# Optimization experiments

Measured on AMD Instinct MI355X. Metric: run time of the kernel, lower is better.

Reference implementation:

```python
import jax, jax.numpy as jnp
import numpy as np

IN, HID, OUT = 64, 256, 64
B, NSTEPS, DELAY = 256, 1024, 20


def setup_inputs() -> dict:
    key = jax.random.key(0)
    ks = jax.random.split(key, 8)
    s = 0.05
    return {
        "input": jax.random.normal(ks[0], (B, NSTEPS, IN), jnp.float32),
        "W_ih_x": jax.random.normal(ks[1], (4 * HID, IN), jnp.float32) * s,
        "W_ih_fb": jax.random.normal(ks[2], (4 * HID, OUT), jnp.float32) * s,
        "W_hh": jax.random.normal(ks[3], (4 * HID, HID), jnp.float32) * s,
        "b_ih": jax.random.normal(ks[4], (4 * HID,), jnp.float32) * s,
        "b_hh": jax.random.normal(ks[5], (4 * HID,), jnp.float32) * s,
        "W_out": jax.random.normal(ks[6], (OUT, HID), jnp.float32) * s,
        "b_out": jax.random.normal(ks[7], (OUT,), jnp.float32) * s,
        "delay": DELAY,
    }


def reference(input, W_ih_x, W_ih_fb, W_hh, b_ih, b_hh, W_out, b_out, delay):
    b, nsteps, _ = input.shape
    H = W_hh.shape[1]
    O = W_out.shape[0]
    # Precompute the input contribution to the gates for all timesteps:
    # gates_t = x_t @ W_ih_x.T + fb @ W_ih_fb.T + h @ W_hh.T + b_ih + b_hh
    xg = jnp.einsum("btd,gd->tbg", input, W_ih_x) + (b_ih + b_hh)  # [T, B, 4H]

    h0 = jnp.zeros((b, H), input.dtype)
    c0 = jnp.zeros((b, H), input.dtype)
    buf0 = jnp.zeros((delay, b, O), input.dtype)  # ring buffer of past outputs
    ptr0 = jnp.zeros((), jnp.int32)

    def step(carry, xg_t):
        h, c, buf, ptr = carry
        fb = buf[ptr]  # output from `delay` steps ago (zeros initially)
        gates = xg_t + fb @ W_ih_fb.T + h @ W_hh.T  # [B, 4H]
        i, f, g, o = jnp.split(gates, 4, axis=-1)  # torch LSTMCell gate order
        c = jax.nn.sigmoid(f) * c + jax.nn.sigmoid(i) * jnp.tanh(g)
        h = jax.nn.sigmoid(o) * jnp.tanh(c)
        out = h @ W_out.T + b_out  # [B, O]
        buf = buf.at[ptr].set(out)
        ptr = (ptr + 1) % delay
        return (h, c, buf, ptr), out

    _, outs = jax.lax.scan(step, (h0, c0, buf0, ptr0), xg)  # outs: [T, B, O]
    return jnp.transpose(outs, (1, 0, 2))  # [B, T, O]
```

## Files before the change

### kernel.cpp

```cpp
#include <hip/hip_runtime.h>


#define BATCH   256
#define TSTEPS  1024
#define IN_DIM  64
#define HID     256
#define OUT_DIM 64
#define DELAY   20
#define CH      8
#define NCH     (TSTEPS / CH)
#define NTHR    512
#define REGP    25

typedef unsigned int u32;
typedef _Float16 half2_t __attribute__((ext_vector_type(2)));

union H2U { u32 u; half2_t h; };
union H1U { unsigned short s; _Float16 h; };

__device__ __forceinline__ u32 pack2(float a, float b) {
    H2U x; x.h = half2_t{(_Float16)a, (_Float16)b}; return x.u;
}
__device__ __forceinline__ unsigned short f16bits(float a) {
    H1U x; x.h = (_Float16)a; return x.s;
}
__device__ __forceinline__ float lo16(u32 u) {
    H1U x; x.s = (unsigned short)(u & 0xffffu); return (float)x.h;
}
__device__ __forceinline__ float hi16(u32 u) {
    H1U x; x.s = (unsigned short)(u >> 16); return (float)x.h;
}
__device__ __forceinline__ float dot2(u32 w, u32 h, float acc) {
    H2U a; a.u = w; H2U b; b.u = h;
    return __builtin_amdgcn_fdot2(a.h, b.h, acc, false);
}
__device__ __forceinline__ float sigm(float x) {
    float e = __expf(-fabsf(x));
    float p = 1.f / (1.f + e);
    return x >= 0.f ? p : 1.f - p;
}
__device__ __forceinline__ float tanh_f(float x) {
    float e = __expf(-2.f * fabsf(x));
    float r = (1.f - e) / (1.f + e);
    return x >= 0.f ? r : -r;
}

#define OFF_WA    0
#define OFF_WB    65536
#define OFF_WC    98304
#define OFF_CB    114688
#define OFF_PART  131072
#define OFF_RING  139264
#define OFF_XF    141824
#define OFF_HG    144000
#define SMEM_BYTES 152192

#define WS_BPK   0
#define WS_WOUT  262144
#define WS_BSUM  294912
#define WS_NEED  299008

__device__ __forceinline__ int orig_row(int gp) {
    return (gp & 3) * 256 + (gp >> 2);
}

__global__ void prepack(const float* __restrict__ Wx,
                        const float* __restrict__ Wfb,
                        const float* __restrict__ Whh,
                        const float* __restrict__ Wout,
                        const float* __restrict__ bih,
                        const float* __restrict__ bhh,
                        uint4* __restrict__ Bpk4,
                        u32* __restrict__ Woutpk,
                        float* __restrict__ bsum_g)
{
    (void)Whh;
    int id = blockIdx.x * 256 + threadIdx.x;
    if (id < 16384) {
        int t = id & 511, rest = id >> 9;
        int kb = rest & 15, j = rest >> 4;
        int r = orig_row(2 * t + j);
        int k0 = kb * 8;
        const float* src = (k0 < 64) ? (Wx + (size_t)r * 64 + k0)
                                     : (Wfb + (size_t)r * 64 + (k0 - 64));
        uint4 v;
        v.x = pack2(src[0], src[1]); v.y = pack2(src[2], src[3]);
        v.z = pack2(src[4], src[5]); v.w = pack2(src[6], src[7]);
        Bpk4[id] = v;
    } else if (id < 16384 + 8192) {
        int s = id - 16384;
        int c = s & 3, o = (s >> 2) & 63, w4 = s >> 8;
        int kp = w4 * 4 + c;
        Woutpk[s] = pack2(Wout[o * HID + 2 * kp], Wout[o * HID + 2 * kp + 1]);
    } else if (id < 16384 + 8192 + 1024) {
        int g = id - 24576;
        int r = orig_row(g);
        bsum_g[g] = bih[r] + bhh[r];
    }
}

__global__ __attribute__((amdgpu_flat_work_group_size(NTHR, NTHR)))
__attribute__((amdgpu_waves_per_eu(2, 2)))
void lstm_persist(const float* __restrict__ input,
                  const float* __restrict__ Whh,
                  const float* __restrict__ bout_g,
                  const uint4* __restrict__ Bpk4,
                  const u32* __restrict__ Woutpk,
                  const float* __restrict__ bsum_g,
                  float* __restrict__ out)
{
    __shared__ alignas(16) unsigned char smem[SMEM_BYTES];
    uint4*          wAl   = (uint4*)(smem + OFF_WA);
    uint2*          wBl   = (uint2*)(smem + OFF_WB);
    u32*            wCl   = (u32*)(smem + OFF_WC);
    u32*            cb32  = (u32*)(smem + OFF_CB);
    unsigned short* part  = (unsigned short*)(smem + OFF_PART);
    unsigned short* ring  = (unsigned short*)(smem + OFF_RING);
    u32*            xfst  = (u32*)(smem + OFF_XF);
    unsigned short* hgs   = (unsigned short*)(smem + OFF_HG);

    const int tid = threadIdx.x;
    const int b   = blockIdx.x;
    const int kq  = tid >> 7;
    const int gl  = tid & 127;

    const float* xin  = input + (size_t)b * TSTEPS * IN_DIM;
    float*       outp = out + (size_t)b * TSTEPS * OUT_DIM;
    const float bo_reg = bout_g[tid & 63];

    u32 wreg[8][REGP];
#pragma unroll
    for (int q = 0; q < 8; ++q) {
        const int r = orig_row(gl * 8 + q);
        const float* wrow = Whh + (size_t)r * HID + kq * 64;
#pragma unroll
        for (int p = 0; p < REGP; ++p) {
            float2 w2 = *(const float2*)(wrow + 2 * p);
            wreg[q][p] = pack2(w2.x, w2.y);
        }
        uint4 av;
        av.x = pack2(wrow[50], wrow[51]); av.y = pack2(wrow[52], wrow[53]);
        av.z = pack2(wrow[54], wrow[55]); av.w = pack2(wrow[56], wrow[57]);
        wAl[q * 512 + tid] = av;
        uint2 bv;
        bv.x = pack2(wrow[58], wrow[59]); bv.y = pack2(wrow[60], wrow[61]);
        wBl[q * 512 + tid] = bv;
        wCl[q * 512 + tid] = pack2(wrow[62], wrow[63]);
    }
    {
        u32* hz = (u32*)hgs;
        hz[tid] = 0u; hz[512 + tid] = 0u; hz[1024 + tid] = 0u; hz[1536 + tid] = 0u;
    }
    __syncthreads();

    float c_state = 0.f;

    auto out_chunk = [&](int tbase) {
        const int lt = tid >> 6, o = tid & 63;
        const int t = tbase + lt;
        const uint4* hrow = (const uint4*)(hgs + (t & 15) * HID);
        const uint4* wp = (const uint4*)Woutpk;
        float a = bo_reg;
        for (int w4 = 0; w4 < 32; ++w4) {
            uint4 wv = wp[w4 * 64 + o];
            uint4 hv = hrow[w4];
            a = dot2(wv.x, hv.x, a); a = dot2(wv.y, hv.y, a);
            a = dot2(wv.z, hv.z, a); a = dot2(wv.w, hv.w, a);
        }
        outp[(size_t)t * OUT_DIM + o] = a;
        ring[(t % DELAY) * 64 + o] = f16bits(a);
    };

#pragma unroll 1
    for (int ch = 0; ch < NCH; ++ch) {
#pragma unroll
        for (int q = 0; q < 8; ++q)
#pragma unroll
            for (int p = 0; p < REGP; ++p)
                asm volatile("" : "+v"(wreg[q][p]));

        const int t0 = ch * CH;
        if (ch > 0) out_chunk(t0 - CH);
        __syncthreads();

        {
            int row = tid >> 6, p = tid & 63;
            int t = t0 + row;
            u32 v;
            if (p < 32) {
                float2 x2 = *(const float2*)(xin + (size_t)t * IN_DIM + 2 * p);
                v = pack2(x2.x, x2.y);
            } else {
                int src = t - DELAY;
                if (src >= 0) {
                    int d = 2 * (p - 32);
                    int sl = src % DELAY;
                    v = (u32)ring[sl * 64 + d] | ((u32)ring[sl * 64 + d + 1] << 16);
                } else v = 0u;
            }
            xfst[row * 68 + p] = v;
        }
        __syncthreads();

        {
            float accA[8], accB[8];
#pragma unroll
            for (int i = 0; i < 8; ++i) { accA[i] = 0.f; accB[i] = 0.f; }
            const uint4* bA = Bpk4 + tid;
            const uint4* bB = Bpk4 + 16 * 512 + tid;
#pragma unroll 1
            for (int kb = 0; kb < 16; ++kb) {
                uint4 wA = bA[kb * 512];
                uint4 wB = bB[kb * 512];
#pragma unroll
                for (int tl = 0; tl < 8; ++tl) {
                    uint4 xv = *(const uint4*)(xfst + tl * 68 + kb * 4);
                    accA[tl] = dot2(wA.x, xv.x, accA[tl]);
                    accA[tl] = dot2(wA.y, xv.y, accA[tl]);
                    accA[tl] = dot2(wA.z, xv.z, accA[tl]);
                    accA[tl] = dot2(wA.w, xv.w, accA[tl]);
                    accB[tl] = dot2(wB.x, xv.x, accB[tl]);
                    accB[tl] = dot2(wB.y, xv.y, accB[tl]);
                    accB[tl] = dot2(wB.z, xv.z, accB[tl]);
                    accB[tl] = dot2(wB.w, xv.w, accB[tl]);
                }
            }
            float2 bs = *(const float2*)(bsum_g + 2 * tid);
#pragma unroll
            for (int tl = 0; tl < 8; ++tl)
                cb32[tl * 512 + tid] = pack2(accA[tl] + bs.x, accB[tl] + bs.y);
        }
        __syncthreads();

#pragma unroll 1
        for (int tl = 0; tl < CH; ++tl) {
            const int t = t0 + tl;
            const u32* hrow = (const u32*)hgs + ((t - 1) & 15) * 128 + kq * 32;

            float acc[8];
            if (kq == 0) {
                uint4 cv = *(const uint4*)(cb32 + tl * 512 + gl * 4);
                acc[0] = lo16(cv.x); acc[1] = hi16(cv.x);
                acc[2] = lo16(cv.y); acc[3] = hi16(cv.y);
                acc[4] = lo16(cv.z); acc[5] = hi16(cv.z);
                acc[6] = lo16(cv.w); acc[7] = hi16(cv.w);
            } else {
#pragma unroll
                for (int q = 0; q < 8; ++q) acc[q] = 0.f;
            }
            {
                uint4 h0 = *(const uint4*)(hrow + 0);
                uint4 h1 = *(const uint4*)(hrow + 4);
                uint4 h2 = *(const uint4*)(hrow + 8);
                uint4 h3 = *(const uint4*)(hrow + 12);
#pragma unroll
                for (int q = 0; q < 8; ++q) {
                    acc[q] = dot2(wreg[q][0],  h0.x, acc[q]);
                    acc[q] = dot2(wreg[q][1],  h0.y, acc[q]);
                    acc[q] = dot2(wreg[q][2],  h0.z, acc[q]);
                    acc[q] = dot2(wreg[q][3],  h0.w, acc[q]);
                    acc[q] = dot2(wreg[q][4],  h1.x, acc[q]);
                    acc[q] = dot2(wreg[q][5],  h1.y, acc[q]);
                    acc[q] = dot2(wreg[q][6],  h1.z, acc[q]);
                    acc[q] = dot2(wreg[q][7],  h1.w, acc[q]);
                    acc[q] = dot2(wreg[q][8],  h2.x, acc[q]);
                    acc[q] = dot2(wreg[q][9],  h2.y, acc[q]);
                    acc[q] = dot2(wreg[q][10], h2.z, acc[q]);
                    acc[q] = dot2(wreg[q][11], h2.w, acc[q]);
                    acc[q] = dot2(wreg[q][12], h3.x, acc[q]);
                    acc[q] = dot2(wreg[q][13], h3.y, acc[q]);
                    acc[q] = dot2(wreg[q][14], h3.z, acc[q]);
                    acc[q] = dot2(wreg[q][15], h3.w, acc[q]);
                }
            }
            {
                uint4 h4 = *(const uint4*)(hrow + 16);
                uint4 h5 = *(const uint4*)(hrow + 20);
                uint4 h6 = *(const uint4*)(hrow + 24);
                uint4 h7 = *(const uint4*)(hrow + 28);
#pragma unroll
                for (int q = 0; q < 8; ++q) {
                    acc[q] = dot2(wreg[q][16], h4.x, acc[q]);
                    acc[q] = dot2(wreg[q][17], h4.y, acc[q]);
                    acc[q] = dot2(wreg[q][18], h4.z, acc[q]);
                    acc[q] = dot2(wreg[q][19], h4.w, acc[q]);
                    acc[q] = dot2(wreg[q][20], h5.x, acc[q]);
                    acc[q] = dot2(wreg[q][21], h5.y, acc[q]);
                    acc[q] = dot2(wreg[q][22], h5.z, acc[q]);
                    acc[q] = dot2(wreg[q][23], h5.w, acc[q]);
                    acc[q] = dot2(wreg[q][24], h6.x, acc[q]);
                    uint4 av = wAl[q * 512 + tid];
                    uint2 bv = wBl[q * 512 + tid];
                    u32   cv = wCl[q * 512 + tid];
                    acc[q] = dot2(av.x, h6.y, acc[q]);
                    acc[q] = dot2(av.y, h6.z, acc[q]);
                    acc[q] = dot2(av.z, h6.w, acc[q]);
                    acc[q] = dot2(av.w, h7.x, acc[q]);
                    acc[q] = dot2(bv.x, h7.y, acc[q]);
                    acc[q] = dot2(bv.y, h7.z, acc[q]);
                    acc[q] = dot2(cv,   h7.w, acc[q]);
                }
            }
            {
                uint4 pw;
                pw.x = pack2(acc[0], acc[1]); pw.y = pack2(acc[2], acc[3]);
                pw.z = pack2(acc[4], acc[5]); pw.w = pack2(acc[6], acc[7]);
                *(uint4*)(part + kq * 1024 + gl * 8) = pw;
            }
            __syncthreads();

            if (tid < 256) {
                float s0 = 0.f, s1 = 0.f, s2 = 0.f, s3 = 0.f;
#pragma unroll
                for (int k = 0; k < 4; ++k) {
                    uint2 rd = *(const uint2*)(part + k * 1024 + tid * 4);
                    s0 += lo16(rd.x); s1 += hi16(rd.x);
                    s2 += lo16(rd.y); s3 += hi16(rd.y);
                }
                c_state = sigm(s1) * c_state + sigm(s0) * tanh_f(s2);
                float hval = sigm(s3) * tanh_f(c_state);
                hgs[(t & 15) * HID + tid] = f16bits(hval);
            }
            __syncthreads();
        }
    }
    out_chunk(TSTEPS - CH);
}

extern "C" void kernel_launch(void* const* d_in, const int* in_sizes, int n_in,
                              void* d_out, int out_size, void* d_ws, size_t ws_size,
                              hipStream_t stream)
{
    (void)in_sizes; (void)n_in; (void)out_size;
    const float* input = (const float*)d_in[0];
    const float* Wx    = (const float*)d_in[1];
    const float* Wfb   = (const float*)d_in[2];
    const float* Whh   = (const float*)d_in[3];
    const float* bih   = (const float*)d_in[4];
    const float* bhh   = (const float*)d_in[5];
    const float* Wo    = (const float*)d_in[6];
    const float* bog   = (const float*)d_in[7];
    float* out = (float*)d_out;

    if (ws_size < (size_t)WS_NEED) return;

    uint4* Bpk4   = (uint4*)((char*)d_ws + WS_BPK);
    u32*   Woutpk = (u32*)((char*)d_ws + WS_WOUT);
    float* bsum_g = (float*)((char*)d_ws + WS_BSUM);

    prepack<<<dim3(100), dim3(256), 0, stream>>>(
        Wx, Wfb, Whh, Wo, bih, bhh, Bpk4, Woutpk, bsum_g);
    lstm_persist<<<dim3(BATCH), dim3(NTHR), 0, stream>>>(
        input, Whh, bog, Bpk4, Woutpk, bsum_g, out);
}
```

Before: 5.031 ms.

## Use MFMA for recurrent and input-gate matmuls with gate-interleaved fragment layout

Replaces the fdot2-based per-thread recurrent matvec and input projection with 16x16x32 f16 MFMA instructions. Recurrent weights are prepacked into MFMA fragment order and held across AGPRs, VGPRs and LDS. The gate layout is arranged so each lane receives all four gates of a unit, which removes the cross-warp partial-sum reduction and one barrier per timestep. The catch is that a batch of one per block uses only one useful column of each 16-wide MFMA, and the pointwise math is duplicated across lanes.

```diff
diff --git a/kernel.cpp b/kernel.cpp
--- a/kernel.cpp
+++ b/kernel.cpp
@@ -10,10 +10,12 @@
 #define CH      8
 #define NCH     (TSTEPS / CH)
 #define NTHR    512
-#define REGP    25
 
 typedef unsigned int u32;
 typedef _Float16 half2_t __attribute__((ext_vector_type(2)));
+typedef _Float16 f16x8 __attribute__((ext_vector_type(8)));
+typedef float    f32x4 __attribute__((ext_vector_type(4)));
+typedef u32      u32x4 __attribute__((ext_vector_type(4)));
 
 union H2U { u32 u; half2_t h; };
 union H1U { unsigned short s; _Float16 h; };
@@ -44,21 +46,23 @@
     float r = (1.f - e) / (1.f + e);
     return x >= 0.f ? r : -r;
 }
-
-#define OFF_WA    0
-#define OFF_WB    65536
-#define OFF_WC    98304
-#define OFF_CB    114688
-#define OFF_PART  131072
-#define OFF_RING  139264
-#define OFF_XF    141824
-#define OFF_HG    144000
-#define SMEM_BYTES 152192
-
-#define WS_BPK   0
-#define WS_WOUT  262144
-#define WS_BSUM  294912
-#define WS_NEED  299008
+__device__ __forceinline__ f32x4 mfma16(u32x4 a, u32x4 b, f32x4 c) {
+    return __builtin_amdgcn_mfma_f32_16x16x32_f16(
+        __builtin_bit_cast(f16x8, a), __builtin_bit_cast(f16x8, b), c, 0, 0, 0);
+}
+
+#define OFF_WLF   0
+#define OFF_CBQ   131072
+#define OFF_RING  147456
+#define OFF_XF    150016
+#define OFF_HG    152192
+#define SMEM_BYTES 160384
+
+#define WS_WHHF  0
+#define WS_BPKF  524288
+#define WS_WOUT  786432
+#define WS_BSUMQ 819200
+#define WS_NEED  823296
 
 __device__ __forceinline__ int orig_row(int gp) {
     return (gp & 3) * 256 + (gp >> 2);
@@ -70,90 +74,104 @@
                         const float* __restrict__ Wout,
                         const float* __restrict__ bih,
                         const float* __restrict__ bhh,
-                        uint4* __restrict__ Bpk4,
+                        uint4* __restrict__ WhhF,
+                        uint4* __restrict__ BpkF,
                         u32* __restrict__ Woutpk,
-                        float* __restrict__ bsum_g)
+                        float4* __restrict__ bsumq)
 {
-    (void)Whh;
     int id = blockIdx.x * 256 + threadIdx.x;
-    if (id < 16384) {
-        int t = id & 511, rest = id >> 9;
-        int kb = rest & 15, j = rest >> 4;
-        int r = orig_row(2 * t + j);
-        int k0 = kb * 8;
-        const float* src = (k0 < 64) ? (Wx + (size_t)r * 64 + k0)
-                                     : (Wfb + (size_t)r * 64 + (k0 - 64));
+    if (id < 32768) {
+        int l = id & 63, ks = (id >> 6) & 7, rb = id >> 9;
+        int r = orig_row(rb * 16 + (l & 15));
+        const float* w = Whh + (size_t)r * HID + ks * 32 + (l >> 4) * 8;
         uint4 v;
-        v.x = pack2(src[0], src[1]); v.y = pack2(src[2], src[3]);
-        v.z = pack2(src[4], src[5]); v.w = pack2(src[6], src[7]);
-        Bpk4[id] = v;
-    } else if (id < 16384 + 8192) {
-        int s = id - 16384;
+        v.x = pack2(w[0], w[1]); v.y = pack2(w[2], w[3]);
+        v.z = pack2(w[4], w[5]); v.w = pack2(w[6], w[7]);
+        WhhF[id] = v;
+    } else if (id < 49152) {
+        int s = id - 32768;
+        int l = s & 63, ks = (s >> 6) & 3, rb = s >> 8;
+        int r = orig_row(rb * 16 + (l & 15));
+        int k0 = ks * 32 + (l >> 4) * 8;
+        float e[8];
+#pragma unroll
+        for (int d = 0; d < 8; ++d) {
+            int k = k0 + d;
+            e[d] = (k < 64) ? Wx[(size_t)r * 64 + k] : Wfb[(size_t)r * 64 + (k - 64)];
+        }
+        uint4 v;
+        v.x = pack2(e[0], e[1]); v.y = pack2(e[2], e[3]);
+        v.z = pack2(e[4], e[5]); v.w = pack2(e[6], e[7]);
+        BpkF[s] = v;
+    } else if (id < 57344) {
+        int s = id - 49152;
         int c = s & 3, o = (s >> 2) & 63, w4 = s >> 8;
         int kp = w4 * 4 + c;
         Woutpk[s] = pack2(Wout[o * HID + 2 * kp], Wout[o * HID + 2 * kp + 1]);
-    } else if (id < 16384 + 8192 + 1024) {
-        int g = id - 24576;
-        int r = orig_row(g);
-        bsum_g[g] = bih[r] + bhh[r];
+    } else if (id < 57600) {
+        int u = id - 57344;
+        float4 bv;
+        bv.x = bih[u]       + bhh[u];
+        bv.y = bih[256 + u] + bhh[256 + u];
+        bv.z = bih[512 + u] + bhh[512 + u];
+        bv.w = bih[768 + u] + bhh[768 + u];
+        bsumq[u] = bv;
     }
 }
 
 __global__ __attribute__((amdgpu_flat_work_group_size(NTHR, NTHR)))
 __attribute__((amdgpu_waves_per_eu(2, 2)))
 void lstm_persist(const float* __restrict__ input,
-                  const float* __restrict__ Whh,
+                  const uint4* __restrict__ WhhF,
+                  const uint4* __restrict__ BpkF,
+                  const u32* __restrict__ Woutpk,
+                  const float4* __restrict__ bsumq,
                   const float* __restrict__ bout_g,
-                  const uint4* __restrict__ Bpk4,
-                  const u32* __restrict__ Woutpk,
-                  const float* __restrict__ bsum_g,
                   float* __restrict__ out)
 {
     __shared__ alignas(16) unsigned char smem[SMEM_BYTES];
-    uint4*          wAl   = (uint4*)(smem + OFF_WA);
-    uint2*          wBl   = (uint2*)(smem + OFF_WB);
-    u32*            wCl   = (u32*)(smem + OFF_WC);
-    u32*            cb32  = (u32*)(smem + OFF_CB);
-    unsigned short* part  = (unsigned short*)(smem + OFF_PART);
+    uint4*          wlf   = (uint4*)(smem + OFF_WLF);
+    uint2*          cbq   = (uint2*)(smem + OFF_CBQ);
     unsigned short* ring  = (unsigned short*)(smem + OFF_RING);
     u32*            xfst  = (u32*)(smem + OFF_XF);
     unsigned short* hgs   = (unsigned short*)(smem + OFF_HG);
 
     const int tid = threadIdx.x;
     const int b   = blockIdx.x;
-    const int kq  = tid >> 7;
-    const int gl  = tid & 127;
+    const int w   = tid >> 6;
+    const int l   = tid & 63;
+    const int kg  = l >> 4;
+    const int col = l & 15;
 
     const float* xin  = input + (size_t)b * TSTEPS * IN_DIM;
     float*       outp = out + (size_t)b * TSTEPS * OUT_DIM;
     const float bo_reg = bout_g[tid & 63];
 
-    u32 wreg[8][REGP];
-#pragma unroll
-    for (int q = 0; q < 8; ++q) {
-        const int r = orig_row(gl * 8 + q);
-        const float* wrow = Whh + (size_t)r * HID + kq * 64;
-#pragma unroll
-        for (int p = 0; p < REGP; ++p) {
-            float2 w2 = *(const float2*)(wrow + 2 * p);
-            wreg[q][p] = pack2(w2.x, w2.y);
-        }
-        uint4 av;
-        av.x = pack2(wrow[50], wrow[51]); av.y = pack2(wrow[52], wrow[53]);
-        av.z = pack2(wrow[54], wrow[55]); av.w = pack2(wrow[56], wrow[57]);
-        wAl[q * 512 + tid] = av;
-        uint2 bv;
-        bv.x = pack2(wrow[58], wrow[59]); bv.y = pack2(wrow[60], wrow[61]);
-        wBl[q * 512 + tid] = bv;
-        wCl[q * 512 + tid] = pack2(wrow[62], wrow[63]);
-    }
+    u32x4 wa[32];
+    u32x4 wv[16];
+#pragma unroll
+    for (int i = 0; i < 32; ++i) {
+        wa[i] = __builtin_bit_cast(u32x4, WhhF[((w * 8 + (i >> 2)) * 8 + (i & 3)) * 64 + l]);
+        asm volatile("" : "+a"(wa[i]));
+    }
+#pragma unroll
+    for (int i = 0; i < 16; ++i) {
+        wv[i] = __builtin_bit_cast(u32x4, WhhF[((w * 8 + (i >> 1)) * 8 + 4 + (i & 1)) * 64 + l]);
+        asm volatile("" : "+v"(wv[i]));
+    }
+#pragma unroll
+    for (int i = 0; i < 16; ++i)
+        wlf[i * 512 + tid] = WhhF[((w * 8 + (i >> 1)) * 8 + 6 + (i & 1)) * 64 + l];
+
     {
         u32* hz = (u32*)hgs;
         hz[tid] = 0u; hz[512 + tid] = 0u; hz[1024 + tid] = 0u; hz[1536 + tid] = 0u;
     }
     __syncthreads();
 
-    float c_state = 0.f;
+    float cst[8];
+#pragma unroll
+    for (int j = 0; j < 8; ++j) cst[j] = 0.f;
 
     auto out_chunk = [&](int tbase) {
         const int lt = tid >> 6, o = tid & 63;
@@ -162,10 +180,10 @@
         const uint4* wp = (const uint4*)Woutpk;
         float a = bo_reg;
         for (int w4 = 0; w4 < 32; ++w4) {
-            uint4 wv = wp[w4 * 64 + o];
+            uint4 wvv = wp[w4 * 64 + o];
             uint4 hv = hrow[w4];
-            a = dot2(wv.x, hv.x, a); a = dot2(wv.y, hv.y, a);
-            a = dot2(wv.z, hv.z, a); a = dot2(wv.w, hv.w, a);
+            a = dot2(wvv.x, hv.x, a); a = dot2(wvv.y, hv.y, a);
+            a = dot2(wvv.z, hv.z, a); a = dot2(wvv.w, hv.w, a);
         }
         outp[(size_t)t * OUT_DIM + o] = a;
         ring[(t % DELAY) * 64 + o] = f16bits(a);
@@ -174,10 +192,9 @@
 #pragma unroll 1
     for (int ch = 0; ch < NCH; ++ch) {
 #pragma unroll
-        for (int q = 0; q < 8; ++q)
-#pragma unroll
-            for (int p = 0; p < REGP; ++p)
-                asm volatile("" : "+v"(wreg[q][p]));
+        for (int i = 0; i < 32; ++i) asm volatile("" : "+a"(wa[i]));
+#pragma unroll
+        for (int i = 0; i < 16; ++i) asm volatile("" : "+v"(wv[i]));
 
         const int t0 = ch * CH;
         if (ch > 0) out_chunk(t0 - CH);
@@ -203,123 +220,76 @@
         __syncthreads();
 
         {
-            float accA[8], accB[8];
-#pragma unroll
-            for (int i = 0; i < 8; ++i) { accA[i] = 0.f; accB[i] = 0.f; }
-            const uint4* bA = Bpk4 + tid;
-            const uint4* bB = Bpk4 + 16 * 512 + tid;
-#pragma unroll 1
-            for (int kb = 0; kb < 16; ++kb) {
-                uint4 wA = bA[kb * 512];
-                uint4 wB = bB[kb * 512];
-#pragma unroll
-                for (int tl = 0; tl < 8; ++tl) {
-                    uint4 xv = *(const uint4*)(xfst + tl * 68 + kb * 4);
-                    accA[tl] = dot2(wA.x, xv.x, accA[tl]);
-                    accA[tl] = dot2(wA.y, xv.y, accA[tl]);
-                    accA[tl] = dot2(wA.z, xv.z, accA[tl]);
-                    accA[tl] = dot2(wA.w, xv.w, accA[tl]);
-                    accB[tl] = dot2(wB.x, xv.x, accB[tl]);
-                    accB[tl] = dot2(wB.y, xv.y, accB[tl]);
-                    accB[tl] = dot2(wB.z, xv.z, accB[tl]);
-                    accB[tl] = dot2(wB.w, xv.w, accB[tl]);
+            const int tc = col & 7;
+            const char* xb_base = (const char*)xfst + tc * 272 + kg * 16;
+#pragma unroll
+            for (int g = 0; g < 2; ++g) {
+                f32x4 ag[4];
+#pragma unroll
+                for (int j = 0; j < 4; ++j) ag[j] = f32x4{0.f, 0.f, 0.f, 0.f};
+#pragma unroll
+                for (int ks = 0; ks < 4; ++ks) {
+                    u32x4 xb = *(const u32x4*)(xb_base + ks * 64);
+#pragma unroll
+                    for (int j = 0; j < 4; ++j) {
+                        const int bb = g * 4 + j;
+                        u32x4 af = __builtin_bit_cast(u32x4,
+                            BpkF[((w * 8 + bb) * 4 + ks) * 64 + l]);
+                        ag[j] = mfma16(af, xb, ag[j]);
+                    }
+                }
+#pragma unroll
+                for (int j = 0; j < 4; ++j) {
+                    const int U = w * 32 + (g * 4 + j) * 4 + kg;
+                    float4 bs = bsumq[U];
+                    if (col < 8) {
+                        uint2 o;
+                        o.x = pack2(ag[j][0] + bs.x, ag[j][1] + bs.y);
+                        o.y = pack2(ag[j][2] + bs.z, ag[j][3] + bs.w);
+                        cbq[U * 8 + col] = o;
+                    }
                 }
             }
-            float2 bs = *(const float2*)(bsum_g + 2 * tid);
-#pragma unroll
-            for (int tl = 0; tl < 8; ++tl)
-                cb32[tl * 512 + tid] = pack2(accA[tl] + bs.x, accB[tl] + bs.y);
         }
         __syncthreads();
 
 #pragma unroll 1
         for (int tl = 0; tl < CH; ++tl) {
             const int t = t0 + tl;
-            const u32* hrow = (const u32*)hgs + ((t - 1) & 15) * 128 + kq * 32;
-
-            float acc[8];
-            if (kq == 0) {
-                uint4 cv = *(const uint4*)(cb32 + tl * 512 + gl * 4);
-                acc[0] = lo16(cv.x); acc[1] = hi16(cv.x);
-                acc[2] = lo16(cv.y); acc[3] = hi16(cv.y);
-                acc[4] = lo16(cv.z); acc[5] = hi16(cv.z);
-                acc[6] = lo16(cv.w); acc[7] = hi16(cv.w);
-            } else {
-#pragma unroll
-                for (int q = 0; q < 8; ++q) acc[q] = 0.f;
-            }
-            {
-                uint4 h0 = *(const uint4*)(hrow + 0);
-                uint4 h1 = *(const uint4*)(hrow + 4);
-                uint4 h2 = *(const uint4*)(hrow + 8);
-                uint4 h3 = *(const uint4*)(hrow + 12);
-#pragma unroll
-                for (int q = 0; q < 8; ++q) {
-                    acc[q] = dot2(wreg[q][0],  h0.x, acc[q]);
-                    acc[q] = dot2(wreg[q][1],  h0.y, acc[q]);
-                    acc[q] = dot2(wreg[q][2],  h0.z, acc[q]);
-                    acc[q] = dot2(wreg[q][3],  h0.w, acc[q]);
-                    acc[q] = dot2(wreg[q][4],  h1.x, acc[q]);
-                    acc[q] = dot2(wreg[q][5],  h1.y, acc[q]);
-                    acc[q] = dot2(wreg[q][6],  h1.z, acc[q]);
-                    acc[q] = dot2(wreg[q][7],  h1.w, acc[q]);
-                    acc[q] = dot2(wreg[q][8],  h2.x, acc[q]);
-                    acc[q] = dot2(wreg[q][9],  h2.y, acc[q]);
-                    acc[q] = dot2(wreg[q][10], h2.z, acc[q]);
-                    acc[q] = dot2(wreg[q][11], h2.w, acc[q]);
-                    acc[q] = dot2(wreg[q][12], h3.x, acc[q]);
-                    acc[q] = dot2(wreg[q][13], h3.y, acc[q]);
-                    acc[q] = dot2(wreg[q][14], h3.z, acc[q]);
-                    acc[q] = dot2(wreg[q][15], h3.w, acc[q]);
+            const char* hb = (const char*)hgs + ((t - 1) & 15) * 512 + kg * 16;
+#pragma unroll
+            for (int g = 0; g < 2; ++g) {
+                f32x4 ac[4];
+#pragma unroll
+                for (int j = 0; j < 4; ++j) ac[j] = f32x4{0.f, 0.f, 0.f, 0.f};
+#pragma unroll
+                for (int ks = 0; ks < 8; ++ks) {
+                    u32x4 hf = *(const u32x4*)(hb + ks * 64);
+#pragma unroll
+                    for (int j = 0; j < 4; ++j) {
+                        const int bb = g * 4 + j;
+                        u32x4 af;
+                        if (ks < 4)      af = wa[bb * 4 + ks];
+                        else if (ks < 6) af = wv[bb * 2 + (ks - 4)];
+                        else             af = __builtin_bit_cast(u32x4,
+                                              wlf[(bb * 2 + (ks - 6)) * 512 + tid]);
+                        ac[j] = mfma16(af, hf, ac[j]);
+                    }
                 }
-            }
-            {
-                uint4 h4 = *(const uint4*)(hrow + 16);
-                uint4 h5 = *(const uint4*)(hrow + 20);
-                uint4 h6 = *(const uint4*)(hrow + 24);
-                uint4 h7 = *(const uint4*)(hrow + 28);
-#pragma unroll
-                for (int q = 0; q < 8; ++q) {
-                    acc[q] = dot2(wreg[q][16], h4.x, acc[q]);
-                    acc[q] = dot2(wreg[q][17], h4.y, acc[q]);
-                    acc[q] = dot2(wreg[q][18], h4.z, acc[q]);
-                    acc[q] = dot2(wreg[q][19], h4.w, acc[q]);
-                    acc[q] = dot2(wreg[q][20], h5.x, acc[q]);
-                    acc[q] = dot2(wreg[q][21], h5.y, acc[q]);
-                    acc[q] = dot2(wreg[q][22], h5.z, acc[q]);
-                    acc[q] = dot2(wreg[q][23], h5.w, acc[q]);
-                    acc[q] = dot2(wreg[q][24], h6.x, acc[q]);
-                    uint4 av = wAl[q * 512 + tid];
-                    uint2 bv = wBl[q * 512 + tid];
-                    u32   cv = wCl[q * 512 + tid];
-                    acc[q] = dot2(av.x, h6.y, acc[q]);
-                    acc[q] = dot2(av.y, h6.z, acc[q]);
-                    acc[q] = dot2(av.z, h6.w, acc[q]);
-                    acc[q] = dot2(av.w, h7.x, acc[q]);
-                    acc[q] = dot2(bv.x, h7.y, acc[q]);
-                    acc[q] = dot2(bv.y, h7.z, acc[q]);
-                    acc[q] = dot2(cv,   h7.w, acc[q]);
+#pragma unroll
+                for (int j = 0; j < 4; ++j) {
+                    const int U = w * 32 + (g * 4 + j) * 4 + kg;
+                    uint2 pre = cbq[U * 8 + tl];
+                    float Si = ac[j][0] + lo16(pre.x);
+                    float Sf = ac[j][1] + hi16(pre.x);
+                    float Sg = ac[j][2] + lo16(pre.y);
+                    float So = ac[j][3] + hi16(pre.y);
+                    const int cj = g * 4 + j;
+                    cst[cj] = sigm(Sf) * cst[cj] + sigm(Si) * tanh_f(Sg);
+                    float hv = sigm(So) * tanh_f(cst[cj]);
+                    if (col == 0)
+                        hgs[(t & 15) * HID + U] = f16bits(hv);
                 }
-            }
-            {
-                uint4 pw;
-                pw.x = pack2(acc[0], acc[1]); pw.y = pack2(acc[2], acc[3]);
-                pw.z = pack2(acc[4], acc[5]); pw.w = pack2(acc[6], acc[7]);
-                *(uint4*)(part + kq * 1024 + gl * 8) = pw;
-            }
-            __syncthreads();
-
-            if (tid < 256) {
-                float s0 = 0.f, s1 = 0.f, s2 = 0.f, s3 = 0.f;
-#pragma unroll
-                for (int k = 0; k < 4; ++k) {
-                    uint2 rd = *(const uint2*)(part + k * 1024 + tid * 4);
-                    s0 += lo16(rd.x); s1 += hi16(rd.x);
-                    s2 += lo16(rd.y); s3 += hi16(rd.y);
-                }
-                c_state = sigm(s1) * c_state + sigm(s0) * tanh_f(s2);
-                float hval = sigm(s3) * tanh_f(c_state);
-                hgs[(t & 15) * HID + tid] = f16bits(hval);
             }
             __syncthreads();
         }
@@ -344,12 +314,13 @@
 
     if (ws_size < (size_t)WS_NEED) return;
 
-    uint4* Bpk4   = (uint4*)((char*)d_ws + WS_BPK);
-    u32*   Woutpk = (u32*)((char*)d_ws + WS_WOUT);
-    float* bsum_g = (float*)((char*)d_ws + WS_BSUM);
-
-    prepack<<<dim3(100), dim3(256), 0, stream>>>(
-        Wx, Wfb, Whh, Wo, bih, bhh, Bpk4, Woutpk, bsum_g);
+    uint4*  WhhF   = (uint4*)((char*)d_ws + WS_WHHF);
+    uint4*  BpkF   = (uint4*)((char*)d_ws + WS_BPKF);
+    u32*    Woutpk = (u32*)((char*)d_ws + WS_WOUT);
+    float4* bsumq  = (float4*)((char*)d_ws + WS_BSUMQ);
+
+    prepack<<<dim3(225), dim3(256), 0, stream>>>(
+        Wx, Wfb, Whh, Wo, bih, bhh, WhhF, BpkF, Woutpk, bsumq);
     lstm_persist<<<dim3(BATCH), dim3(NTHR), 0, stream>>>(
-        input, Whh, bog, Bpk4, Woutpk, bsum_g, out);
-}
+        input, WhhF, BpkF, Woutpk, bsumq, bog, out);
+}
```

Result: slower. 8.349 ms (+65.9%).
